# Kernel tuning notes

Hardware: AMD Instinct MI355X
Metric: run time of the kernel (lower is better)

The kernel has to match this reference:

```python
import jax, jax.numpy as jnp
import numpy as np

N_CAT = 10000   # n_categories
E = 128         # embedding_dim_c
D = 4           # n_demand
H = 128         # hidden_size
B = 32          # batch_size
S = 50          # max_session_len
I = 5000        # n_items (candidate pool)


def setup_inputs() -> dict:
    key = jax.random.key(0)
    ks = jax.random.split(key, 7)
    inp = jax.random.randint(ks[0], (B, S), 0, N_CAT)
    cand = jax.random.randint(ks[1], (I,), 0, N_CAT)
    emb_table = jax.random.normal(ks[2], (N_CAT, E), jnp.float32) * 0.02
    emb_table = emb_table.at[0].set(0.0)  # padding_idx=0
    W_demand = jax.random.normal(ks[3], (D * H, E), jnp.float32) / np.float32(np.sqrt(E))
    W_score = jax.random.normal(ks[4], (H, 2 * H), jnp.float32) / np.float32(np.sqrt(2 * H))  # torch [out,in]
    b_score = jax.random.normal(ks[5], (H,), jnp.float32) * 0.01
    w_score = jax.random.uniform(ks[6], (H,), jnp.float32, 0.0, 1.0 / np.float32(np.sqrt(H)))
    return {"input": inp, "candidate_pool_category": cand, "emb_table": emb_table,
            "W_demand": W_demand, "W_score": W_score, "b_score": b_score, "w_score": w_score}


def _forward(input, candidate_pool_category, emb_table, W_demand, W_score, b_score, w_score):
    h = w_score.shape[0]
    d = W_demand.shape[0] // h
    b, s = input.shape
    emb = emb_table[input]                                   # [B,S,E]
    hidden = (emb @ W_demand.T).reshape(b, s, d, h)          # [B,S,D,H] (hidden_key == hidden_demand)
    # demand_agg == 'exp': log(sum(exp(.), axis=seq))
    agg = jnp.log(jnp.sum(jnp.exp(hidden), axis=1))          # [B,D,H]
    # demand similarity loss: mean off-diagonal pairwise cosine similarity (batch-averaged)
    nrm = jnp.maximum(jnp.linalg.norm(agg, axis=-1, keepdims=True), 1e-8)
    u = agg / nrm
    gram = jnp.mean(jnp.einsum('bdh,beh->bde', u, u), axis=0)  # [D,D]
    off = 1.0 - jnp.eye(d, dtype=gram.dtype)
    demand_sim_loss = jnp.sum(gram * off) / (d * (d - 1))
    # split score Linear weight into demand/key halves (concat order: (agg, key))
    Wd, Wk = W_score[:, :h], W_score[:, h:]                  # each [H, H]
    agg_proj = agg @ Wd.T + b_score                          # [B,D,H]
    key_proj = jnp.einsum('bsdh,oh->bsdo', hidden, Wk)       # [B,S,D,H]
    demand_score = jnp.einsum('bsdh,h->bds',
                              jax.nn.relu(agg_proj[:, None] + key_proj), w_score)  # [B,D,S]
    cand_emb = emb_table[candidate_pool_category]            # [I,E]
    cand_hidden = (cand_emb @ W_demand.T).reshape(-1, d, h)  # [I,D,H]
    cand_proj = jnp.einsum('idh,oh->ido', cand_hidden, Wk)   # [I,D,H]
    demand_score_candidate = jnp.einsum('bdih,h->bdi',
                                        jax.nn.relu(agg_proj[:, :, None, :] + jnp.transpose(cand_proj, (1, 0, 2))[None]),
                                        w_score)             # [B,D,I]
    # score_act_fun is None -> no activation
    return demand_score, demand_score_candidate, emb, cand_emb, demand_sim_loss


def reference(input, candidate_pool_category, emb_table, W_demand, W_score, b_score, w_score):
    return _forward(input, candidate_pool_category, emb_table, W_demand, W_score, b_score, w_score)
```

## Files before the change

kernel.cpp:

```cpp
#include <hip/hip_runtime.h>

typedef __attribute__((ext_vector_type(8))) short short8;
typedef __attribute__((ext_vector_type(16))) float f32x16;

#define NROWS_IN 1600
#define NI 5000
#define BB 32
#define DDk 4
#define SS 50

__device__ __forceinline__ unsigned short f2bf(float f) {
    unsigned int u = __float_as_uint(f);
    u = (u + 0x7FFFu + ((u >> 16) & 1u)) >> 16;
    return (unsigned short)u;
}
__device__ __forceinline__ float b2f(unsigned short u) {
    return __uint_as_float(((unsigned int)u) << 16);
}

__global__ __launch_bounds__(256) void k_prep(const int* __restrict__ inp,
                                              const int* __restrict__ cand,
                                              const float* __restrict__ et,
                                              const float* __restrict__ Wd,
                                              const float* __restrict__ Ws,
                                              unsigned short* __restrict__ Wcat,
                                              unsigned short* __restrict__ Abf,
                                              float* __restrict__ o_emb,
                                              float* __restrict__ o_cemb) {
    int t = threadIdx.x;
    int blk = blockIdx.x;
    if (blk < 16) {
        const float4* src = (const float4*)Wd;
#pragma unroll
        for (int q = 0; q < 4; ++q) {
            int i = blk * 256 + t + q * 4096;
            float4 v = src[i];
            ushort4 o;
            o.x = f2bf(v.x); o.y = f2bf(v.y); o.z = f2bf(v.z); o.w = f2bf(v.w);
            *(ushort4*)(Wcat + (size_t)i * 4) = o;
        }
        return;
    }
    if (blk < 80) {
        __shared__ __align__(16) float sdw[128 * 128];
        __shared__ float wk[8][128];
        int cb = blk - 16;
        int d = cb >> 4, ot = cb & 15;
        const float4* src = (const float4*)(Wd + (size_t)d * 128 * 128);
#pragma unroll
        for (int q = 0; q < 16; ++q) {
            int i = t + q * 256;
            *(float4*)(&sdw[i * 4]) = src[i];
        }
        for (int x = t; x < 8 * 128; x += 256) {
            int ol = x >> 7, h = x & 127;
            wk[ol][h] = Ws[(ot * 8 + ol) * 256 + 128 + h];
        }
        __syncthreads();
        int e = t & 127, og = t >> 7;
        float acc[4] = {0.f, 0.f, 0.f, 0.f};
        for (int h = 0; h < 128; ++h) {
            float rd = sdw[h * 128 + e];
#pragma unroll
            for (int k = 0; k < 4; ++k) acc[k] += rd * wk[og * 4 + k][h];
        }
#pragma unroll
        for (int k = 0; k < 4; ++k) {
            int o = ot * 8 + og * 4 + k;
            Wcat[(size_t)(512 + d * 128 + o) * 128 + e] = f2bf(acc[k]);
        }
        return;
    }
    int pb = blk - 80;
    int r = pb * 8 + (t >> 5);
    int fc = t & 31;
    int id = (r < NROWS_IN) ? inp[r] : cand[r - NROWS_IN];
    float4 v = *(const float4*)(et + (size_t)id * 128 + fc * 4);
    if (r < NROWS_IN) *(float4*)(o_emb + (size_t)r * 128 + fc * 4) = v;
    else              *(float4*)(o_cemb + (size_t)(r - NROWS_IN) * 128 + fc * 4) = v;
    ushort4 o;
    o.x = f2bf(v.x); o.y = f2bf(v.y); o.z = f2bf(v.z); o.w = f2bf(v.w);
    *(ushort4*)(Abf + (size_t)r * 128 + fc * 4) = o;
}

__global__ __launch_bounds__(256) void k_fused_mid(const unsigned short* __restrict__ Abf,
                                                   const unsigned short* __restrict__ Wcat,
                                                   const float* __restrict__ Ws,
                                                   const float* __restrict__ bsc,
                                                   const float* __restrict__ wsc,
                                                   float* __restrict__ aggw,
                                                   float* __restrict__ apw,
                                                   float* __restrict__ o_ds) {
    __shared__ __align__(16) char lds[37152];
    unsigned short* sb   = (unsigned short*)lds;
    float*          skp  = (float*)lds;
    float*          sred = (float*)(lds + 32768);
    float*          sagg = (float*)(lds + 35328);
    float*          sap  = (float*)(lds + 35840);
    float*          spart= (float*)(lds + 36352);

    int b = blockIdx.x >> 2, d = blockIdx.x & 3;
    int t = threadIdx.x;
    int w = t >> 6, lane = t & 63;
    int lr = lane & 31, g = lane >> 5;
    int rt = w & 1, ct = w >> 1;
    int arow = rt * 32 + lr;

    short8 a8[8];
    {
        const unsigned short* arp = Abf + (size_t)(b * SS + arow) * 128;
#pragma unroll
        for (int ks = 0; ks < 8; ++ks) {
            short8 v = {0, 0, 0, 0, 0, 0, 0, 0};
            if (arow < SS) v = *(const short8*)(arp + (ks * 2 + g) * 8);
            a8[ks] = v;
        }
    }
#pragma unroll
    for (int q = 0; q < 8; ++q) {
        int x = t + q * 256;
        int r = x >> 4, ch = x & 15;
        short8 v = *(const short8*)(Wcat + (size_t)(d * 128 + r) * 128 + ch * 8);
        *(short8*)(sb + r * 128 + ((ch ^ (r & 15)) << 3)) = v;
    }
    __syncthreads();

    int bcol0 = ct * 64 + lr, bcol1 = ct * 64 + 32 + lr;
    const unsigned short* pb0 = sb + bcol0 * 128;
    const unsigned short* pb1 = sb + bcol1 * 128;
    int b0x = bcol0 & 15, b1x = bcol1 & 15;
    f32x16 h0 = {}, h1 = {};
#pragma unroll
    for (int ks = 0; ks < 8; ++ks) {
        int chA = ks * 2 + g;
        short8 b8 = *(const short8*)(pb0 + ((chA ^ b0x) << 3));
        short8 c8 = *(const short8*)(pb1 + ((chA ^ b1x) << 3));
        h0 = __builtin_amdgcn_mfma_f32_32x32x16_bf16(a8[ks], b8, h0, 0, 0, 0);
        h1 = __builtin_amdgcn_mfma_f32_32x32x16_bf16(a8[ks], c8, h1, 0, 0, 0);
    }
    float p0 = 0.f, p1 = 0.f;
#pragma unroll
    for (int r = 0; r < 16; ++r) {
        int row = rt * 32 + (r & 3) + 8 * (r >> 2) + 4 * g;
        if (row < SS) { p0 += expf(h0[r]); p1 += expf(h1[r]); }
    }
    sred[bcol0 * 5 + rt * 2 + g] = p0;
    sred[bcol1 * 5 + rt * 2 + g] = p1;
    __syncthreads();
#pragma unroll
    for (int q = 0; q < 8; ++q) {
        int x = t + q * 256;
        int r = x >> 4, ch = x & 15;
        short8 v = *(const short8*)(Wcat + (size_t)(512 + d * 128 + r) * 128 + ch * 8);
        *(short8*)(sb + r * 128 + ((ch ^ (r & 15)) << 3)) = v;
    }
    if (t < 128) {
        float s = sred[t * 5] + sred[t * 5 + 1] + sred[t * 5 + 2] + sred[t * 5 + 3];
        float a = logf(s);
        sagg[t] = a;
        aggw[b * 512 + d * 128 + t] = a;
    }
    __syncthreads();
    f32x16 k0 = {}, k1 = {};
#pragma unroll
    for (int ks = 0; ks < 8; ++ks) {
        int chA = ks * 2 + g;
        short8 b8 = *(const short8*)(pb0 + ((chA ^ b0x) << 3));
        short8 c8 = *(const short8*)(pb1 + ((chA ^ b1x) << 3));
        k0 = __builtin_amdgcn_mfma_f32_32x32x16_bf16(a8[ks], b8, k0, 0, 0, 0);
        k1 = __builtin_amdgcn_mfma_f32_32x32x16_bf16(a8[ks], c8, k1, 0, 0, 0);
    }
    if (t < 128) {
        const float* wr = Ws + t * 256;
        float acc = bsc[t];
        for (int ch = 0; ch < 32; ++ch) {
            float4 a4 = *(const float4*)(sagg + ch * 4);
            float4 w4 = *(const float4*)(wr + ch * 4);
            acc += a4.x * w4.x + a4.y * w4.y + a4.z * w4.z + a4.w * w4.w;
        }
        sap[t] = acc;
        apw[(b * DDk + d) * 128 + t] = acc;
    }
    __syncthreads();
#pragma unroll
    for (int r = 0; r < 16; ++r) {
        int row = rt * 32 + (r & 3) + 8 * (r >> 2) + 4 * g;
        int c0 = ct * 64 + lr, c1 = ct * 64 + 32 + lr;
        skp[row * 128 + ((((c0 >> 2) ^ (row & 7)) << 2) | (c0 & 3))] = k0[r];
        skp[row * 128 + ((((c1 >> 2) ^ (row & 7)) << 2) | (c1 & 3))] = k1[r];
    }
    __syncthreads();
    if (t < 200) {
        int s = t >> 2, oq = t & 3;
        float acc = 0.f;
#pragma unroll
        for (int c = 0; c < 8; ++c) {
            int ch = oq * 8 + c;
            float4 a4 = *(const float4*)(sap + ch * 4);
            float4 w4 = *(const float4*)(wsc + ch * 4);
            float4 k4 = *(const float4*)(&skp[s * 128 + ((ch ^ (s & 7)) << 2)]);
            acc += w4.x * fmaxf(a4.x + k4.x, 0.f) + w4.y * fmaxf(a4.y + k4.y, 0.f)
                 + w4.z * fmaxf(a4.z + k4.z, 0.f) + w4.w * fmaxf(a4.w + k4.w, 0.f);
        }
        spart[t] = acc;
    }
    __syncthreads();
    if (t < SS) {
        float v = spart[t * 4] + spart[t * 4 + 1] + spart[t * 4 + 2] + spart[t * 4 + 3];
        o_ds[b * (DDk * SS) + d * SS + t] = v;
    }
}

__global__ __launch_bounds__(256) void k_cand(const unsigned short* __restrict__ Abf,
                                              const unsigned short* __restrict__ Wcat,
                                              const float* __restrict__ apw,
                                              const float* __restrict__ aggw,
                                              const float* __restrict__ wsc,
                                              float* __restrict__ o_dsc,
                                              float* __restrict__ o_loss) {
    __shared__ __align__(16) char lds[49664];
    int gid = blockIdx.x;
    int t = threadIdx.x;
    if (gid >= 316) {
        float* nrm = (float*)lds;
        if (t < 128) {
            const float* a = aggw + t * 128;
            float s = 0.f;
            for (int h = 0; h < 128; ++h) s += a[h] * a[h];
            nrm[t] = fmaxf(sqrtf(s), 1e-8f);
        }
        __syncthreads();
        float lb = 0.f;
        if (t < 32) {
            const float* a = aggw + t * 512;
            float i0 = 1.f / nrm[t * 4 + 0], i1 = 1.f / nrm[t * 4 + 1];
            float i2 = 1.f / nrm[t * 4 + 2], i3 = 1.f / nrm[t * 4 + 3];
            for (int h = 0; h < 128; ++h) {
                float u0 = a[h] * i0, u1 = a[128 + h] * i1;
                float u2 = a[256 + h] * i2, u3 = a[384 + h] * i3;
                float v = u0 + u1 + u2 + u3;
                lb += v * v - (u0 * u0 + u1 * u1 + u2 * u2 + u3 * u3);
            }
        }
        for (int off = 32; off; off >>= 1) lb += __shfl_down(lb, off);
        if (t == 0) o_loss[0] = lb / (float)(BB * DDk * (DDk - 1));
        return;
    }
    unsigned short* sw    = (unsigned short*)lds;
    unsigned short* scp16 = (unsigned short*)lds;
    float*          sap   = (float*)(lds + 32768);
    float*          swv   = (float*)(lds + 49152);

    int tile = gid >> 2, d = gid & 3;
    int i0 = tile * 64;
    int w = t >> 6, lane = t & 63;
    int rbase = (w & 1) * 32, cbase = (w >> 1) * 64;
    int lr = lane & 31, g = lane >> 5;
    int arow = rbase + lr;

    short8 a8[8];
    {
        const unsigned short* arp = Abf + (size_t)(NROWS_IN + i0 + arow) * 128;
        bool valid = (i0 + arow < NI);
#pragma unroll
        for (int ks = 0; ks < 8; ++ks) {
            short8 v = {0, 0, 0, 0, 0, 0, 0, 0};
            if (valid) v = *(const short8*)(arp + (ks * 2 + g) * 8);
            a8[ks] = v;
        }
    }
#pragma unroll
    for (int q = 0; q < 8; ++q) {
        int x = t + q * 256;
        int r = x >> 4, ch = x & 15;
        short8 v = *(const short8*)(Wcat + (size_t)(512 + d * 128 + r) * 128 + ch * 8);
        *(short8*)(sw + r * 128 + ((ch ^ (r & 15)) << 3)) = v;
    }
    if (t < 128) swv[t] = wsc[t];
#pragma unroll
    for (int q = 0; q < 4; ++q) {
        int x = t + q * 256;
        int b = x >> 5, ch = x & 31;
        float4 v = *(const float4*)(apw + (size_t)(b * 4 + d) * 128 + ch * 4);
        *(float4*)(&sap[b * 128 + ((ch ^ (b & 7)) << 2)]) = v;
    }
    __syncthreads();
    int bcol0 = cbase + lr, bcol1 = cbase + 32 + lr;
    const unsigned short* pb0 = sw + bcol0 * 128;
    const unsigned short* pb1 = sw + bcol1 * 128;
    int b0x = bcol0 & 15, b1x = bcol1 & 15;
    f32x16 acc0 = {}, acc1 = {};
#pragma unroll
    for (int ks = 0; ks < 8; ++ks) {
        int chA = ks * 2 + g;
        short8 b8 = *(const short8*)(pb0 + ((chA ^ b0x) << 3));
        short8 c8 = *(const short8*)(pb1 + ((chA ^ b1x) << 3));
        acc0 = __builtin_amdgcn_mfma_f32_32x32x16_bf16(a8[ks], b8, acc0, 0, 0, 0);
        acc1 = __builtin_amdgcn_mfma_f32_32x32x16_bf16(a8[ks], c8, acc1, 0, 0, 0);
    }
    __syncthreads();
#pragma unroll
    for (int r = 0; r < 16; ++r) {
        int row = rbase + (r & 3) + 8 * (r >> 2) + 4 * g;
        int c0 = cbase + lr, c1 = cbase + 32 + lr;
        scp16[row * 128 + ((((c0 >> 2) ^ (row & 31)) << 2) | (c0 & 3))] = f2bf(acc0[r]);
        scp16[row * 128 + ((((c1 >> 2) ^ (row & 31)) << 2) | (c1 & 3))] = f2bf(acc1[r]);
    }
    __syncthreads();
    int b2 = t >> 4, gg = t & 15;
    float accA0 = 0.f, accA1 = 0.f, accA2 = 0.f, accA3 = 0.f;
    float accB0 = 0.f, accB1 = 0.f, accB2 = 0.f, accB3 = 0.f;
    const float* sapA = sap + b2 * 128;
    const float* sapB = sap + (b2 + 16) * 128;
    int bx = b2 & 7;
    for (int ch = 0; ch < 32; ++ch) {
        float4 w4 = *(const float4*)(swv + ch * 4);
        float4 aA = *(const float4*)(sapA + ((ch ^ bx) << 2));
        float4 aB = *(const float4*)(sapB + ((ch ^ bx) << 2));
#pragma unroll
        for (int kk = 0; kk < 4; ++kk) {
            int il = kk * 16 + gg;
            ushort4 cc = *(const ushort4*)(scp16 + il * 128 + ((ch ^ (il & 31)) << 2));
            float c0 = b2f(cc.x), c1 = b2f(cc.y), c2 = b2f(cc.z), c3 = b2f(cc.w);
            float pA = w4.x * fmaxf(aA.x + c0, 0.f) + w4.y * fmaxf(aA.y + c1, 0.f)
                     + w4.z * fmaxf(aA.z + c2, 0.f) + w4.w * fmaxf(aA.w + c3, 0.f);
            float pB = w4.x * fmaxf(aB.x + c0, 0.f) + w4.y * fmaxf(aB.y + c1, 0.f)
                     + w4.z * fmaxf(aB.z + c2, 0.f) + w4.w * fmaxf(aB.w + c3, 0.f);
            if (kk == 0) { accA0 += pA; accB0 += pB; }
            else if (kk == 1) { accA1 += pA; accB1 += pB; }
            else if (kk == 2) { accA2 += pA; accB2 += pB; }
            else { accA3 += pA; accB3 += pB; }
        }
    }
    {
        size_t baseA = (size_t)b2 * (DDk * NI) + d * NI;
        size_t baseB = (size_t)(b2 + 16) * (DDk * NI) + d * NI;
        int ia = i0 + gg;
        if (ia < NI)      { o_dsc[baseA + ia]      = accA0; o_dsc[baseB + ia]      = accB0; }
        if (ia + 16 < NI) { o_dsc[baseA + ia + 16] = accA1; o_dsc[baseB + ia + 16] = accB1; }
        if (ia + 32 < NI) { o_dsc[baseA + ia + 32] = accA2; o_dsc[baseB + ia + 32] = accB2; }
        if (ia + 48 < NI) { o_dsc[baseA + ia + 48] = accA3; o_dsc[baseB + ia + 48] = accB3; }
    }
}

extern "C" void kernel_launch(void* const* d_in, const int* in_sizes, int n_in,
                              void* d_out, int out_size, void* d_ws, size_t ws_size,
                              hipStream_t stream) {
    const int*   inp  = (const int*)d_in[0];
    const int*   cand = (const int*)d_in[1];
    const float* et   = (const float*)d_in[2];
    const float* Wd   = (const float*)d_in[3];
    const float* Ws   = (const float*)d_in[4];
    const float* bsc  = (const float*)d_in[5];
    const float* wsc  = (const float*)d_in[6];

    float* out = (float*)d_out;
    float* o_ds   = out;
    float* o_dsc  = out + 6400;
    float* o_emb  = out + 646400;
    float* o_cemb = out + 851200;
    float* o_loss = out + 1491200;

    char* wsb = (char*)d_ws;
    unsigned short* Wcat = (unsigned short*)wsb;
    unsigned short* Abf  = (unsigned short*)(wsb + 262144);
    float* aggw = (float*)(wsb + 2097152);
    float* apw  = aggw + 16384;

    hipLaunchKernelGGL(k_prep, dim3(905), dim3(256), 0, stream,
                       inp, cand, et, Wd, Ws, Wcat, Abf, o_emb, o_cemb);
    hipLaunchKernelGGL(k_fused_mid, dim3(128), dim3(256), 0, stream,
                       Abf, Wcat, Ws, bsc, wsc, aggw, apw, o_ds);
    hipLaunchKernelGGL(k_cand, dim3(317), dim3(256), 0, stream,
                       Abf, Wcat, apw, aggw, wsc, o_dsc, o_loss);
}
```

Baseline: 38.86 us.

## Split candidate scoring across batch groups and widen the mid kernel to 512 threads

Result: slower. 40.93 us (+5.3%).

```diff
diff --git a/kernel.cpp b/kernel.cpp
--- a/kernel.cpp
+++ b/kernel.cpp
@@ -8,6 +8,7 @@
 #define BB 32
 #define DDk 4
 #define SS 50
+#define NTILES 79
 
 __device__ __forceinline__ unsigned short f2bf(float f) {
     unsigned int u = __float_as_uint(f);
@@ -83,7 +84,7 @@
     *(ushort4*)(Abf + (size_t)r * 128 + fc * 4) = o;
 }
 
-__global__ __launch_bounds__(256) void k_fused_mid(const unsigned short* __restrict__ Abf,
+__global__ __launch_bounds__(512) void k_fused_mid(const unsigned short* __restrict__ Abf,
                                                    const unsigned short* __restrict__ Wcat,
                                                    const float* __restrict__ Ws,
                                                    const float* __restrict__ bsc,
@@ -117,39 +118,35 @@
         }
     }
 #pragma unroll
-    for (int q = 0; q < 8; ++q) {
-        int x = t + q * 256;
+    for (int q = 0; q < 4; ++q) {
+        int x = t + q * 512;
         int r = x >> 4, ch = x & 15;
         short8 v = *(const short8*)(Wcat + (size_t)(d * 128 + r) * 128 + ch * 8);
         *(short8*)(sb + r * 128 + ((ch ^ (r & 15)) << 3)) = v;
     }
     __syncthreads();
 
-    int bcol0 = ct * 64 + lr, bcol1 = ct * 64 + 32 + lr;
-    const unsigned short* pb0 = sb + bcol0 * 128;
-    const unsigned short* pb1 = sb + bcol1 * 128;
-    int b0x = bcol0 & 15, b1x = bcol1 & 15;
-    f32x16 h0 = {}, h1 = {};
+    int bcol = ct * 32 + lr;
+    const unsigned short* pb = sb + bcol * 128;
+    int bx = bcol & 15;
+    f32x16 h0 = {};
 #pragma unroll
     for (int ks = 0; ks < 8; ++ks) {
         int chA = ks * 2 + g;
-        short8 b8 = *(const short8*)(pb0 + ((chA ^ b0x) << 3));
-        short8 c8 = *(const short8*)(pb1 + ((chA ^ b1x) << 3));
+        short8 b8 = *(const short8*)(pb + ((chA ^ bx) << 3));
         h0 = __builtin_amdgcn_mfma_f32_32x32x16_bf16(a8[ks], b8, h0, 0, 0, 0);
-        h1 = __builtin_amdgcn_mfma_f32_32x32x16_bf16(a8[ks], c8, h1, 0, 0, 0);
-    }
-    float p0 = 0.f, p1 = 0.f;
+    }
+    float p0 = 0.f;
 #pragma unroll
     for (int r = 0; r < 16; ++r) {
         int row = rt * 32 + (r & 3) + 8 * (r >> 2) + 4 * g;
-        if (row < SS) { p0 += expf(h0[r]); p1 += expf(h1[r]); }
-    }
-    sred[bcol0 * 5 + rt * 2 + g] = p0;
-    sred[bcol1 * 5 + rt * 2 + g] = p1;
-    __syncthreads();
-#pragma unroll
-    for (int q = 0; q < 8; ++q) {
-        int x = t + q * 256;
+        if (row < SS) p0 += expf(h0[r]);
+    }
+    sred[bcol * 5 + rt * 2 + g] = p0;
+    __syncthreads();
+#pragma unroll
+    for (int q = 0; q < 4; ++q) {
+        int x = t + q * 512;
         int r = x >> 4, ch = x & 15;
         short8 v = *(const short8*)(Wcat + (size_t)(512 + d * 128 + r) * 128 + ch * 8);
         *(short8*)(sb + r * 128 + ((ch ^ (r & 15)) << 3)) = v;
@@ -161,14 +158,12 @@
         aggw[b * 512 + d * 128 + t] = a;
     }
     __syncthreads();
-    f32x16 k0 = {}, k1 = {};
+    f32x16 k0 = {};
 #pragma unroll
     for (int ks = 0; ks < 8; ++ks) {
         int chA = ks * 2 + g;
-        short8 b8 = *(const short8*)(pb0 + ((chA ^ b0x) << 3));
-        short8 c8 = *(const short8*)(pb1 + ((chA ^ b1x) << 3));
+        short8 b8 = *(const short8*)(pb + ((chA ^ bx) << 3));
         k0 = __builtin_amdgcn_mfma_f32_32x32x16_bf16(a8[ks], b8, k0, 0, 0, 0);
-        k1 = __builtin_amdgcn_mfma_f32_32x32x16_bf16(a8[ks], c8, k1, 0, 0, 0);
     }
     if (t < 128) {
         const float* wr = Ws + t * 256;
@@ -185,9 +180,8 @@
 #pragma unroll
     for (int r = 0; r < 16; ++r) {
         int row = rt * 32 + (r & 3) + 8 * (r >> 2) + 4 * g;
-        int c0 = ct * 64 + lr, c1 = ct * 64 + 32 + lr;
+        int c0 = ct * 32 + lr;
         skp[row * 128 + ((((c0 >> 2) ^ (row & 7)) << 2) | (c0 & 3))] = k0[r];
-        skp[row * 128 + ((((c1 >> 2) ^ (row & 7)) << 2) | (c1 & 3))] = k1[r];
     }
     __syncthreads();
     if (t < 200) {
@@ -218,10 +212,10 @@
                                               const float* __restrict__ wsc,
                                               float* __restrict__ o_dsc,
                                               float* __restrict__ o_loss) {
-    __shared__ __align__(16) char lds[49664];
+    __shared__ __align__(16) char lds[37376];
     int gid = blockIdx.x;
     int t = threadIdx.x;
-    if (gid >= 316) {
+    if (gid >= NTILES * 16) {
         float* nrm = (float*)lds;
         if (t < 128) {
             const float* a = aggw + t * 128;
@@ -246,12 +240,14 @@
         if (t == 0) o_loss[0] = lb / (float)(BB * DDk * (DDk - 1));
         return;
     }
-    unsigned short* sw    = (unsigned short*)lds;
-    unsigned short* scp16 = (unsigned short*)lds;
-    float*          sap   = (float*)(lds + 32768);
-    float*          swv   = (float*)(lds + 49152);
-
-    int tile = gid >> 2, d = gid & 3;
+    unsigned short* sw  = (unsigned short*)lds;
+    float*          scp = (float*)lds;
+    float*          sap = (float*)(lds + 32768);
+    float*          swv = (float*)(lds + 36864);
+
+    int tile = gid >> 4;
+    int sub = gid & 15;
+    int d = sub >> 2, bg = sub & 3;
     int i0 = tile * 64;
     int w = t >> 6, lane = t & 63;
     int rbase = (w & 1) * 32, cbase = (w >> 1) * 64;
@@ -277,12 +273,10 @@
         *(short8*)(sw + r * 128 + ((ch ^ (r & 15)) << 3)) = v;
     }
     if (t < 128) swv[t] = wsc[t];
-#pragma unroll
-    for (int q = 0; q < 4; ++q) {
-        int x = t + q * 256;
-        int b = x >> 5, ch = x & 31;
-        float4 v = *(const float4*)(apw + (size_t)(b * 4 + d) * 128 + ch * 4);
-        *(float4*)(&sap[b * 128 + ((ch ^ (b & 7)) << 2)]) = v;
+    {
+        int bi = t >> 5, ch = t & 31;
+        float4 v = *(const float4*)(apw + (size_t)((bg * 8 + bi) * 4 + d) * 128 + ch * 4);
+        *(float4*)(&sap[bi * 128 + ((ch ^ (bi & 7)) << 2)]) = v;
     }
     __syncthreads();
     int bcol0 = cbase + lr, bcol1 = cbase + 32 + lr;
@@ -303,43 +297,28 @@
     for (int r = 0; r < 16; ++r) {
         int row = rbase + (r & 3) + 8 * (r >> 2) + 4 * g;
         int c0 = cbase + lr, c1 = cbase + 32 + lr;
-        scp16[row * 128 + ((((c0 >> 2) ^ (row & 31)) << 2) | (c0 & 3))] = f2bf(acc0[r]);
-        scp16[row * 128 + ((((c1 >> 2) ^ (row & 31)) << 2) | (c1 & 3))] = f2bf(acc1[r]);
-    }
-    __syncthreads();
-    int b2 = t >> 4, gg = t & 15;
-    float accA0 = 0.f, accA1 = 0.f, accA2 = 0.f, accA3 = 0.f;
-    float accB0 = 0.f, accB1 = 0.f, accB2 = 0.f, accB3 = 0.f;
-    const float* sapA = sap + b2 * 128;
-    const float* sapB = sap + (b2 + 16) * 128;
-    int bx = b2 & 7;
+        scp[row * 128 + ((((c0 >> 2) ^ (row & 31)) << 2) | (c0 & 3))] = acc0[r];
+        scp[row * 128 + ((((c1 >> 2) ^ (row & 31)) << 2) | (c1 & 3))] = acc1[r];
+    }
+    __syncthreads();
+    int bo = t >> 5, gg = t & 31;
+    float accA = 0.f, accB = 0.f;
+    const float* sapA = sap + bo * 128;
     for (int ch = 0; ch < 32; ++ch) {
         float4 w4 = *(const float4*)(swv + ch * 4);
-        float4 aA = *(const float4*)(sapA + ((ch ^ bx) << 2));
-        float4 aB = *(const float4*)(sapB + ((ch ^ bx) << 2));
-#pragma unroll
-        for (int kk = 0; kk < 4; ++kk) {
-            int il = kk * 16 + gg;
-            ushort4 cc = *(const ushort4*)(scp16 + il * 128 + ((ch ^ (il & 31)) << 2));
-            float c0 = b2f(cc.x), c1 = b2f(cc.y), c2 = b2f(cc.z), c3 = b2f(cc.w);
-            float pA = w4.x * fmaxf(aA.x + c0, 0.f) + w4.y * fmaxf(aA.y + c1, 0.f)
-                     + w4.z * fmaxf(aA.z + c2, 0.f) + w4.w * fmaxf(aA.w + c3, 0.f);
-            float pB = w4.x * fmaxf(aB.x + c0, 0.f) + w4.y * fmaxf(aB.y + c1, 0.f)
-                     + w4.z * fmaxf(aB.z + c2, 0.f) + w4.w * fmaxf(aB.w + c3, 0.f);
-            if (kk == 0) { accA0 += pA; accB0 += pB; }
-            else if (kk == 1) { accA1 += pA; accB1 += pB; }
-            else if (kk == 2) { accA2 += pA; accB2 += pB; }
-            else { accA3 += pA; accB3 += pB; }
-        }
+        float4 a4 = *(const float4*)(sapA + ((ch ^ bo) << 2));
+        float4 cA = *(const float4*)(&scp[gg * 128 + ((ch ^ gg) << 2)]);
+        float4 cB = *(const float4*)(&scp[(32 + gg) * 128 + ((ch ^ gg) << 2)]);
+        accA += w4.x * fmaxf(a4.x + cA.x, 0.f) + w4.y * fmaxf(a4.y + cA.y, 0.f)
+              + w4.z * fmaxf(a4.z + cA.z, 0.f) + w4.w * fmaxf(a4.w + cA.w, 0.f);
+        accB += w4.x * fmaxf(a4.x + cB.x, 0.f) + w4.y * fmaxf(a4.y + cB.y, 0.f)
+              + w4.z * fmaxf(a4.z + cB.z, 0.f) + w4.w * fmaxf(a4.w + cB.w, 0.f);
     }
     {
-        size_t baseA = (size_t)b2 * (DDk * NI) + d * NI;
-        size_t baseB = (size_t)(b2 + 16) * (DDk * NI) + d * NI;
+        size_t base = (size_t)(bg * 8 + bo) * (DDk * NI) + d * NI;
         int ia = i0 + gg;
-        if (ia < NI)      { o_dsc[baseA + ia]      = accA0; o_dsc[baseB + ia]      = accB0; }
-        if (ia + 16 < NI) { o_dsc[baseA + ia + 16] = accA1; o_dsc[baseB + ia + 16] = accB1; }
-        if (ia + 32 < NI) { o_dsc[baseA + ia + 32] = accA2; o_dsc[baseB + ia + 32] = accB2; }
-        if (ia + 48 < NI) { o_dsc[baseA + ia + 48] = accA3; o_dsc[baseB + ia + 48] = accB3; }
+        if (ia < NI)      o_dsc[base + ia]      = accA;
+        if (ia + 32 < NI) o_dsc[base + ia + 32] = accB;
     }
 }
 
@@ -369,8 +348,8 @@
 
     hipLaunchKernelGGL(k_prep, dim3(905), dim3(256), 0, stream,
                        inp, cand, et, Wd, Ws, Wcat, Abf, o_emb, o_cemb);
-    hipLaunchKernelGGL(k_fused_mid, dim3(128), dim3(256), 0, stream,
+    hipLaunchKernelGGL(k_fused_mid, dim3(128), dim3(512), 0, stream,
                        Abf, Wcat, Ws, bsc, wsc, aggw, apw, o_ds);
-    hipLaunchKernelGGL(k_cand, dim3(317), dim3(256), 0, stream,
+    hipLaunchKernelGGL(k_cand, dim3(NTILES * 16 + 1), dim3(256), 0, stream,
                        Abf, Wcat, apw, aggw, wsc, o_dsc, o_loss);
 }
```
